# Optimization experiments

Measured on AMD Instinct MI355X. Metric: run time of the kernel, lower is better.

The kernel has to match this reference:

```python
import jax, jax.numpy as jnp
import numpy as np

N_SPK, N_UTT, D = 1024, 32, 128
EPS = 1e-8  # matches F.cosine_similarity eps


def setup_inputs() -> dict:
    key = jax.random.key(0)
    emb = jax.random.normal(key, (N_SPK * N_UTT, D), dtype=jnp.float32)
    emb = emb / jnp.linalg.norm(emb, axis=-1, keepdims=True)  # L2-normalized per docstring
    return {
        "embeddings": emb,
        "w": jnp.asarray(10.0, dtype=jnp.float32),
        "b": jnp.asarray(-5.0, dtype=jnp.float32),
        "n_speakers": N_SPK,
        "n_utterances": N_UTT,
    }


def reference(embeddings, w, b, n_speakers, n_utterances):
    # [N, M, D]
    e = embeddings.reshape(n_speakers, n_utterances, -1)
    cent = e.mean(axis=1)  # [N, D] full centroids
    # exclusive centroids: mean over all utterances except i -> [N, M, D]
    cent_excl = (e.sum(axis=1, keepdims=True) - e) / (n_utterances - 1)

    e_n = jnp.maximum(jnp.linalg.norm(e, axis=-1), EPS)          # [N, M]
    c_n = jnp.maximum(jnp.linalg.norm(cent, axis=-1), EPS)       # [N]
    ce_n = jnp.maximum(jnp.linalg.norm(cent_excl, axis=-1), EPS) # [N, M]

    # cosine sim of every utterance vs every full centroid: [N, M, N]
    sim = jnp.einsum('nmd,kd->nmk', e, cent) / (e_n[:, :, None] * c_n[None, None, :])
    # own-speaker entry uses the exclusive centroid instead
    sim_own = jnp.sum(e * cent_excl, axis=-1) / (e_n * ce_n)     # [N, M]
    eye = jnp.eye(n_speakers, dtype=bool)[:, None, :]            # [N, 1, N]
    sim = jnp.where(eye, sim_own[:, :, None], sim)

    logits = (w * sim + b).reshape(n_speakers * n_utterances, n_speakers)
    targets = jnp.repeat(jnp.arange(n_speakers), n_utterances)
    logp = jax.nn.log_softmax(logits, axis=-1)
    loss = -jnp.take_along_axis(logp, targets[:, None], axis=-1).mean()
    return loss
```

## Files before the change

### kernel.cpp

```cpp
#include <hip/hip_runtime.h>
#include <math.h>

#define NSPK 1024
#define NUTT 32
#define DIM  128
#define NROWS (NSPK * NUTT)
#define EPS 1e-8f
#define LOG2E 1.44269504f

typedef __attribute__((ext_vector_type(8))) short short8;
typedef __attribute__((ext_vector_type(4))) float floatx4;

__device__ inline unsigned short f2bf(float f) {
  union { float f; unsigned u; } v; v.f = f;
  unsigned r = v.u + 0x7fffu + ((v.u >> 16) & 1u);
  return (unsigned short)(r >> 16);
}

__global__ __launch_bounds__(256) void k_prep(const float* __restrict__ emb,
                                              const float* __restrict__ wp,
                                              const float* __restrict__ bp,
                                              unsigned short* __restrict__ centN,
                                              float* __restrict__ rs2,
                                              float* __restrict__ eol,
                                              float* __restrict__ olv) {
  __shared__ __align__(16) float E[32 * 132];
  __shared__ __align__(16) float Sl[128];
  __shared__ float red2[2];

  int n = blockIdx.x, t = threadIdx.x;

  const float4* e4 = (const float4*)emb + (size_t)n * 1024;
#pragma unroll
  for (int i = 0; i < 4; ++i) {
    int idx4 = t + 256 * i;
    int m = idx4 >> 5, d4 = (idx4 & 31) << 2;
    *(float4*)&E[m * 132 + d4] = e4[idx4];
  }
  __syncthreads();

  float s = 0.f;
  if (t < 128) {
    for (int m = 0; m < 32; ++m) s += E[m * 132 + t];
    Sl[t] = s;
    float p = s * s;
#pragma unroll
    for (int mask = 1; mask < 64; mask <<= 1) p += __shfl_xor(p, mask, 64);
    if ((t & 63) == 0) red2[t >> 6] = p;
  }
  __syncthreads();
  float ss = red2[0] + red2[1];

  if (t < 128) {
    float cn = fmaxf(sqrtf(ss) * (1.0f / NUTT), EPS);
    centN[(size_t)n * DIM + t] = f2bf(s / (NUTT * cn));
  }

  int row = t >> 3, sub = t & 7;
  float ee = 0.f, es = 0.f;
  int base = row * 132 + sub * 16;
#pragma unroll
  for (int i = 0; i < 4; ++i) {
    float4 ev = *(const float4*)&E[base + i * 4];
    float4 sv = *(const float4*)&Sl[sub * 16 + i * 4];
    ee += ev.x * ev.x + ev.y * ev.y + ev.z * ev.z + ev.w * ev.w;
    es += ev.x * sv.x + ev.y * sv.y + ev.z * sv.z + ev.w * sv.w;
  }
#pragma unroll
  for (int mask = 1; mask < 8; mask <<= 1) {
    ee += __shfl_xor(ee, mask, 64);
    es += __shfl_xor(es, mask, 64);
  }
  if (sub == 0) {
    float w = wp[0], b = bp[0];
    float M = b + fabsf(w);
    float en = fmaxf(sqrtf(ee), EPS);
    float dot_own = (es - ee) * (1.0f / (NUTT - 1));
    float ex2 = (ss - 2.0f * es + ee) * (1.0f / ((NUTT - 1) * (NUTT - 1)));
    float cen = fmaxf(sqrtf(ex2), EPS);
    float ol = w * dot_own / (en * cen) + b;
    int r = n * NUTT + row;
    olv[r] = ol;
    eol[r] = exp2f((ol - M) * LOG2E);
    rs2[r] = w * LOG2E / en;
  }
}

__global__ __launch_bounds__(256, 2) void k_mfma(const float* __restrict__ emb,
                                                 const unsigned short* __restrict__ centN,
                                                 const float* __restrict__ rs2g,
                                                 const float* __restrict__ eolg,
                                                 const float* __restrict__ olvg,
                                                 const float* __restrict__ wp,
                                                 const float* __restrict__ bp,
                                                 float* __restrict__ out) {
  __shared__ __align__(16) unsigned short A[64 * 136];
  __shared__ float sPart[4 * 64];

  int b = blockIdx.x, t = threadIdx.x;
  int wid = t >> 6, lane = t & 63;
  int lg = lane >> 4, lc = lane & 15;
  int s0 = b * 2;

  const float4* e4 = (const float4*)emb + (size_t)b * 2048;
#pragma unroll
  for (int i = 0; i < 8; ++i) {
    int idx4 = t + 256 * i;
    int lr = idx4 >> 5, d4 = (idx4 & 31) << 2;
    float4 v = e4[idx4];
    ushort4 bv;
    bv.x = f2bf(v.x); bv.y = f2bf(v.y); bv.z = f2bf(v.z); bv.w = f2bf(v.w);
    *(ushort4*)&A[lr * 136 + d4] = bv;
  }
  __syncthreads();

  short8 af[4][4];
#pragma unroll
  for (int rt = 0; rt < 4; ++rt)
#pragma unroll
    for (int ks = 0; ks < 4; ++ks)
      af[rt][ks] = *(const short8*)&A[(rt * 16 + lc) * 136 + ks * 32 + lg * 8];

  float rsL[16], eolL[16];
#pragma unroll
  for (int rt = 0; rt < 4; ++rt) {
    float4 r4 = *(const float4*)&rs2g[b * 64 + rt * 16 + lg * 4];
    float4 o4 = *(const float4*)&eolg[b * 64 + rt * 16 + lg * 4];
    rsL[rt * 4 + 0] = r4.x; rsL[rt * 4 + 1] = r4.y; rsL[rt * 4 + 2] = r4.z; rsL[rt * 4 + 3] = r4.w;
    eolL[rt * 4 + 0] = o4.x; eolL[rt * 4 + 1] = o4.y; eolL[rt * 4 + 2] = o4.z; eolL[rt * 4 + 3] = o4.w;
  }

  float w = wp[0], bb = bp[0];
  float M = bb + fabsf(w);
  float c2 = (bb - M) * LOG2E;

  float sAcc[16];
#pragma unroll
  for (int j = 0; j < 16; ++j) sAcc[j] = 0.f;

  int colbase = wid * 256;
#pragma unroll 2
  for (int ct = 0; ct < 16; ++ct) {
    int c0 = colbase + ct * 16;
    int col = c0 + lc;
    const short8* bptr = (const short8*)(centN + (size_t)col * DIM + lg * 8);
    short8 bf[4];
#pragma unroll
    for (int ks = 0; ks < 4; ++ks) bf[ks] = bptr[ks * 4];

    floatx4 acc[4];
#pragma unroll
    for (int rt = 0; rt < 4; ++rt) acc[rt] = (floatx4){0.f, 0.f, 0.f, 0.f};
#pragma unroll
    for (int ks = 0; ks < 4; ++ks)
#pragma unroll
      for (int rt = 0; rt < 4; ++rt)
        acc[rt] = __builtin_amdgcn_mfma_f32_16x16x32_bf16(af[rt][ks], bf[ks], acc[rt], 0, 0, 0);

    bool fix = (unsigned)(s0 - c0) < 16u;
#pragma unroll
    for (int rt = 0; rt < 4; ++rt) {
      int own = s0 + (rt >> 1);
#pragma unroll
      for (int reg = 0; reg < 4; ++reg) {
        float l2 = fmaf(rsL[rt * 4 + reg], acc[rt][reg], c2);
        float e = exp2f(l2);
        if (fix && col == own) e = eolL[rt * 4 + reg];
        sAcc[rt * 4 + reg] += e;
      }
    }
  }

#pragma unroll
  for (int mask = 1; mask < 16; mask <<= 1)
#pragma unroll
    for (int j = 0; j < 16; ++j) sAcc[j] += __shfl_xor(sAcc[j], mask, 64);

  if (lc == 0)
#pragma unroll
    for (int rt = 0; rt < 4; ++rt)
#pragma unroll
      for (int reg = 0; reg < 4; ++reg)
        sPart[wid * 64 + rt * 16 + lg * 4 + reg] = sAcc[rt * 4 + reg];
  __syncthreads();

  if (t < 64) {
    float st = sPart[t] + sPart[64 + t] + sPart[128 + t] + sPart[192 + t];
    float lossr = M + logf(st) - olvg[b * 64 + t];
#pragma unroll
    for (int mask = 1; mask < 64; mask <<= 1) lossr += __shfl_xor(lossr, mask, 64);
    if (t == 0) atomicAdd(out, lossr * (1.0f / NROWS));
  }
}

extern "C" void kernel_launch(void* const* d_in, const int* in_sizes, int n_in,
                              void* d_out, int out_size, void* d_ws, size_t ws_size,
                              hipStream_t stream) {
  const float* emb = (const float*)d_in[0];
  const float* wp  = (const float*)d_in[1];
  const float* bp  = (const float*)d_in[2];

  char* ws = (char*)d_ws;
  unsigned short* centN = (unsigned short*)ws;
  float* rs2 = (float*)(ws + 262144);
  float* eol = (float*)(ws + 262144 + 131072);
  float* olv = (float*)(ws + 262144 + 262144);
  float* out = (float*)d_out;

  hipMemsetAsync(d_out, 0, sizeof(float), stream);
  hipLaunchKernelGGL(k_prep, dim3(NSPK), dim3(256), 0, stream,
                     emb, wp, bp, centN, rs2, eol, olv);
  hipLaunchKernelGGL(k_mfma, dim3(NSPK / 2), dim3(256), 0, stream,
                     emb, centN, rs2, eol, olv, wp, bp, out);
}
```

Before: 98.25 us.

## Fuse prep and MFMA kernels into one cooperative launch with grid sync

Merges the centroid/prep kernel and the MFMA softmax kernel into a single cooperative kernel of 512 blocks. Each block preps its own two speakers, keeping per-row scalars and the bf16 A tile in shared memory, then grid-syncs before the similarity pass. A second grid sync replaces the memset and atomics with a deterministic final reduction. The B-fragment loads are also software-prefetched one column tile ahead. The aim is to remove launch gaps, the memset and the global round-trip of per-row data, at the cost of two grid-wide barriers and a startup probe with a fallback two-kernel path.

```diff
diff --git a/kernel.cpp b/kernel.cpp
--- a/kernel.cpp
+++ b/kernel.cpp
@@ -1,5 +1,8 @@
 #include <hip/hip_runtime.h>
+#include <hip/hip_cooperative_groups.h>
 #include <math.h>
+
+namespace cg = cooperative_groups;
 
 #define NSPK 1024
 #define NUTT 32
@@ -17,102 +20,82 @@
   return (unsigned short)(r >> 16);
 }
 
-__global__ __launch_bounds__(256) void k_prep(const float* __restrict__ emb,
-                                              const float* __restrict__ wp,
-                                              const float* __restrict__ bp,
-                                              unsigned short* __restrict__ centN,
-                                              float* __restrict__ rs2,
-                                              float* __restrict__ eol,
-                                              float* __restrict__ olv) {
-  __shared__ __align__(16) float E[32 * 132];
-  __shared__ __align__(16) float Sl[128];
-  __shared__ float red2[2];
-
-  int n = blockIdx.x, t = threadIdx.x;
-
-  const float4* e4 = (const float4*)emb + (size_t)n * 1024;
-#pragma unroll
-  for (int i = 0; i < 4; ++i) {
-    int idx4 = t + 256 * i;
-    int m = idx4 >> 5, d4 = (idx4 & 31) << 2;
-    *(float4*)&E[m * 132 + d4] = e4[idx4];
+__device__ __forceinline__ void phase1(
+    int b, int t, const float* __restrict__ emb, float w, float bb, float M,
+    unsigned short* __restrict__ centN, float* __restrict__ rs2g,
+    float* __restrict__ eolg, float* __restrict__ olvg,
+    float* Sl, float* red, float* rowRS, float* rowEOL, float* rowOLV,
+    unsigned short* A) {
+  int sp = t >> 7, d = t & 127;
+  {
+    const float* eb = emb + (size_t)(b * 2 + sp) * NUTT * DIM + d;
+    float s = 0.f;
+#pragma unroll
+    for (int m = 0; m < NUTT; ++m) s += eb[m * DIM];
+    Sl[sp * 128 + d] = s;
+    float p = s * s;
+#pragma unroll
+    for (int mask = 1; mask < 64; mask <<= 1) p += __shfl_xor(p, mask, 64);
+    if ((t & 63) == 0) red[t >> 6] = p;
   }
   __syncthreads();
-
-  float s = 0.f;
-  if (t < 128) {
-    for (int m = 0; m < 32; ++m) s += E[m * 132 + t];
-    Sl[t] = s;
-    float p = s * s;
-#pragma unroll
-    for (int mask = 1; mask < 64; mask <<= 1) p += __shfl_xor(p, mask, 64);
-    if ((t & 63) == 0) red2[t >> 6] = p;
-  }
-  __syncthreads();
-  float ss = red2[0] + red2[1];
-
-  if (t < 128) {
+  float ss0 = red[0] + red[1], ss1 = red[2] + red[3];
+
+  {
+    float ss = sp ? ss1 : ss0;
+    float s = Sl[sp * 128 + d];
     float cn = fmaxf(sqrtf(ss) * (1.0f / NUTT), EPS);
-    centN[(size_t)n * DIM + t] = f2bf(s / (NUTT * cn));
-  }
-
-  int row = t >> 3, sub = t & 7;
-  float ee = 0.f, es = 0.f;
-  int base = row * 132 + sub * 16;
-#pragma unroll
-  for (int i = 0; i < 4; ++i) {
-    float4 ev = *(const float4*)&E[base + i * 4];
-    float4 sv = *(const float4*)&Sl[sub * 16 + i * 4];
-    ee += ev.x * ev.x + ev.y * ev.y + ev.z * ev.z + ev.w * ev.w;
-    es += ev.x * sv.x + ev.y * sv.y + ev.z * sv.z + ev.w * sv.w;
-  }
-#pragma unroll
-  for (int mask = 1; mask < 8; mask <<= 1) {
-    ee += __shfl_xor(ee, mask, 64);
-    es += __shfl_xor(es, mask, 64);
-  }
-  if (sub == 0) {
-    float w = wp[0], b = bp[0];
-    float M = b + fabsf(w);
-    float en = fmaxf(sqrtf(ee), EPS);
-    float dot_own = (es - ee) * (1.0f / (NUTT - 1));
-    float ex2 = (ss - 2.0f * es + ee) * (1.0f / ((NUTT - 1) * (NUTT - 1)));
-    float cen = fmaxf(sqrtf(ex2), EPS);
-    float ol = w * dot_own / (en * cen) + b;
-    int r = n * NUTT + row;
-    olv[r] = ol;
-    eol[r] = exp2f((ol - M) * LOG2E);
-    rs2[r] = w * LOG2E / en;
-  }
-}
-
-__global__ __launch_bounds__(256, 2) void k_mfma(const float* __restrict__ emb,
-                                                 const unsigned short* __restrict__ centN,
-                                                 const float* __restrict__ rs2g,
-                                                 const float* __restrict__ eolg,
-                                                 const float* __restrict__ olvg,
-                                                 const float* __restrict__ wp,
-                                                 const float* __restrict__ bp,
-                                                 float* __restrict__ out) {
-  __shared__ __align__(16) unsigned short A[64 * 136];
-  __shared__ float sPart[4 * 64];
-
-  int b = blockIdx.x, t = threadIdx.x;
-  int wid = t >> 6, lane = t & 63;
-  int lg = lane >> 4, lc = lane & 15;
-  int s0 = b * 2;
-
-  const float4* e4 = (const float4*)emb + (size_t)b * 2048;
+    centN[(size_t)(b * 2 + sp) * DIM + d] = f2bf(s / (NUTT * cn));
+  }
+
+  {
+    int row = t >> 2, sub = t & 3;
+    int rsp = row >> 5;
+    const float* er = emb + (size_t)(b * 64 + row) * DIM + sub * 32;
+    const float* Srow = &Sl[rsp * 128 + sub * 32];
+    float ee = 0.f, es = 0.f;
+#pragma unroll
+    for (int i = 0; i < 8; ++i) {
+      float4 ev = *(const float4*)&er[i * 4];
+      float4 sv = *(const float4*)&Srow[i * 4];
+      ee += ev.x * ev.x + ev.y * ev.y + ev.z * ev.z + ev.w * ev.w;
+      es += ev.x * sv.x + ev.y * sv.y + ev.z * sv.z + ev.w * sv.w;
+    }
+    ee += __shfl_xor(ee, 1, 64); es += __shfl_xor(es, 1, 64);
+    ee += __shfl_xor(ee, 2, 64); es += __shfl_xor(es, 2, 64);
+    if (sub == 0) {
+      float ss = rsp ? ss1 : ss0;
+      float en = fmaxf(sqrtf(ee), EPS);
+      float dot_own = (es - ee) * (1.0f / (NUTT - 1));
+      float ex2 = (ss - 2.f * es + ee) * (1.0f / ((NUTT - 1) * (NUTT - 1)));
+      float cen = fmaxf(sqrtf(ex2), EPS);
+      float ol = w * dot_own / (en * cen) + bb;
+      float eo = exp2f((ol - M) * LOG2E);
+      float rs = w * LOG2E / en;
+      int gr = b * 64 + row;
+      rowOLV[row] = ol; olvg[gr] = ol;
+      rowEOL[row] = eo; eolg[gr] = eo;
+      rowRS[row] = rs;  rs2g[gr] = rs;
+    }
+  }
+
 #pragma unroll
   for (int i = 0; i < 8; ++i) {
     int idx4 = t + 256 * i;
-    int lr = idx4 >> 5, d4 = (idx4 & 31) << 2;
-    float4 v = e4[idx4];
+    int r = idx4 >> 5, d4 = (idx4 & 31) << 2;
+    float4 v = *(const float4*)(emb + (size_t)b * 8192 + (size_t)idx4 * 4);
     ushort4 bv;
     bv.x = f2bf(v.x); bv.y = f2bf(v.y); bv.z = f2bf(v.z); bv.w = f2bf(v.w);
-    *(ushort4*)&A[lr * 136 + d4] = bv;
-  }
-  __syncthreads();
+    *(ushort4*)&A[r * 136 + d4] = bv;
+  }
+}
+
+__device__ __forceinline__ float phase2(
+    int b, int t, const unsigned short* __restrict__ centN,
+    const unsigned short* A, const float* rowRS, const float* rowEOL,
+    const float* rowOLV, float M, float c2, float* sPart) {
+  int wid = t >> 6, lane = t & 63, lg = lane >> 4, lc = lane & 15;
+  int s0 = b * 2;
 
   short8 af[4][4];
 #pragma unroll
@@ -124,30 +107,31 @@
   float rsL[16], eolL[16];
 #pragma unroll
   for (int rt = 0; rt < 4; ++rt) {
-    float4 r4 = *(const float4*)&rs2g[b * 64 + rt * 16 + lg * 4];
-    float4 o4 = *(const float4*)&eolg[b * 64 + rt * 16 + lg * 4];
+    float4 r4 = *(const float4*)&rowRS[rt * 16 + lg * 4];
+    float4 o4 = *(const float4*)&rowEOL[rt * 16 + lg * 4];
     rsL[rt * 4 + 0] = r4.x; rsL[rt * 4 + 1] = r4.y; rsL[rt * 4 + 2] = r4.z; rsL[rt * 4 + 3] = r4.w;
     eolL[rt * 4 + 0] = o4.x; eolL[rt * 4 + 1] = o4.y; eolL[rt * 4 + 2] = o4.z; eolL[rt * 4 + 3] = o4.w;
   }
 
-  float w = wp[0], bb = bp[0];
-  float M = bb + fabsf(w);
-  float c2 = (bb - M) * LOG2E;
-
   float sAcc[16];
 #pragma unroll
   for (int j = 0; j < 16; ++j) sAcc[j] = 0.f;
 
   int colbase = wid * 256;
-#pragma unroll 2
+  int col0 = colbase + lc;
+  const short8* cb8 = (const short8*)centN;
+
+  short8 bcur[4], bnxt[4];
+  {
+    const short8* p = cb8 + (size_t)col0 * 16 + lg;
+    bcur[0] = p[0]; bcur[1] = p[4]; bcur[2] = p[8]; bcur[3] = p[12];
+  }
+
   for (int ct = 0; ct < 16; ++ct) {
-    int c0 = colbase + ct * 16;
-    int col = c0 + lc;
-    const short8* bptr = (const short8*)(centN + (size_t)col * DIM + lg * 8);
-    short8 bf[4];
-#pragma unroll
-    for (int ks = 0; ks < 4; ++ks) bf[ks] = bptr[ks * 4];
-
+    if (ct < 15) {
+      const short8* p = cb8 + (size_t)(col0 + (ct + 1) * 16) * 16 + lg;
+      bnxt[0] = p[0]; bnxt[1] = p[4]; bnxt[2] = p[8]; bnxt[3] = p[12];
+    }
     floatx4 acc[4];
 #pragma unroll
     for (int rt = 0; rt < 4; ++rt) acc[rt] = (floatx4){0.f, 0.f, 0.f, 0.f};
@@ -155,8 +139,9 @@
     for (int ks = 0; ks < 4; ++ks)
 #pragma unroll
       for (int rt = 0; rt < 4; ++rt)
-        acc[rt] = __builtin_amdgcn_mfma_f32_16x16x32_bf16(af[rt][ks], bf[ks], acc[rt], 0, 0, 0);
-
+        acc[rt] = __builtin_amdgcn_mfma_f32_16x16x32_bf16(af[rt][ks], bcur[ks], acc[rt], 0, 0, 0);
+
+    int c0 = colbase + ct * 16, col = c0 + lc;
     bool fix = (unsigned)(s0 - c0) < 16u;
 #pragma unroll
     for (int rt = 0; rt < 4; ++rt) {
@@ -169,6 +154,8 @@
         sAcc[rt * 4 + reg] += e;
       }
     }
+#pragma unroll
+    for (int ks = 0; ks < 4; ++ks) bcur[ks] = bnxt[ks];
   }
 
 #pragma unroll
@@ -184,13 +171,168 @@
         sPart[wid * 64 + rt * 16 + lg * 4 + reg] = sAcc[rt * 4 + reg];
   __syncthreads();
 
+  float blockSum = 0.f;
   if (t < 64) {
     float st = sPart[t] + sPart[64 + t] + sPart[128 + t] + sPart[192 + t];
-    float lossr = M + logf(st) - olvg[b * 64 + t];
+    float lossr = M + logf(st) - rowOLV[t];
 #pragma unroll
     for (int mask = 1; mask < 64; mask <<= 1) lossr += __shfl_xor(lossr, mask, 64);
-    if (t == 0) atomicAdd(out, lossr * (1.0f / NROWS));
-  }
+    blockSum = lossr;
+  }
+  return blockSum;
+}
+
+__global__ __launch_bounds__(256, 2) void k_fused(const float* __restrict__ emb,
+                                                  const float* __restrict__ wp,
+                                                  const float* __restrict__ bp,
+                                                  unsigned short* __restrict__ centN,
+                                                  float* __restrict__ rs2g,
+                                                  float* __restrict__ eolg,
+                                                  float* __restrict__ olvg,
+                                                  float* __restrict__ partial,
+                                                  float* __restrict__ out) {
+  __shared__ __align__(16) unsigned short A[64 * 136];
+  __shared__ __align__(16) float Sl[2 * 128];
+  __shared__ float red[4];
+  __shared__ __align__(16) float rowRS[64], rowEOL[64], rowOLV[64];
+  __shared__ __align__(16) float sPart[256];
+
+  int b = blockIdx.x, t = threadIdx.x;
+  float w = wp[0], bb = bp[0];
+  float M = bb + fabsf(w);
+  float c2 = -fabsf(w) * LOG2E;
+
+  phase1(b, t, emb, w, bb, M, centN, rs2g, eolg, olvg,
+         Sl, red, rowRS, rowEOL, rowOLV, A);
+
+  __threadfence();
+  cg::this_grid().sync();
+
+  float v = phase2(b, t, centN, A, rowRS, rowEOL, rowOLV, M, c2, sPart);
+  if (t == 0) partial[b] = v;
+
+  __threadfence();
+  cg::this_grid().sync();
+
+  if (b == 0) {
+    float s = partial[t] + partial[t + 256];
+#pragma unroll
+    for (int mask = 1; mask < 64; mask <<= 1) s += __shfl_xor(s, mask, 64);
+    __syncthreads();
+    if ((t & 63) == 0) red[t >> 6] = s;
+    __syncthreads();
+    if (t == 0) out[0] = (red[0] + red[1] + red[2] + red[3]) * (1.0f / NROWS);
+  }
+}
+
+__global__ __launch_bounds__(256) void k_prep_fb(const float* __restrict__ emb,
+                                                 const float* __restrict__ wp,
+                                                 const float* __restrict__ bp,
+                                                 unsigned short* __restrict__ centN,
+                                                 float* __restrict__ rs2g,
+                                                 float* __restrict__ eolg,
+                                                 float* __restrict__ olvg,
+                                                 float* __restrict__ out) {
+  __shared__ __align__(16) unsigned short A[64 * 136];
+  __shared__ __align__(16) float Sl[2 * 128];
+  __shared__ float red[4];
+  __shared__ __align__(16) float rowRS[64], rowEOL[64], rowOLV[64];
+  int b = blockIdx.x, t = threadIdx.x;
+  float w = wp[0], bb = bp[0];
+  float M = bb + fabsf(w);
+  if (b == 0 && t == 0) out[0] = 0.f;
+  phase1(b, t, emb, w, bb, M, centN, rs2g, eolg, olvg,
+         Sl, red, rowRS, rowEOL, rowOLV, A);
+}
+
+__global__ __launch_bounds__(256, 2) void k_mfma_fb(const float* __restrict__ emb,
+                                                    const unsigned short* __restrict__ centN,
+                                                    const float* __restrict__ rs2g,
+                                                    const float* __restrict__ eolg,
+                                                    const float* __restrict__ olvg,
+                                                    const float* __restrict__ wp,
+                                                    const float* __restrict__ bp,
+                                                    float* __restrict__ out) {
+  __shared__ __align__(16) unsigned short A[64 * 136];
+  __shared__ __align__(16) float rowRS[64], rowEOL[64], rowOLV[64];
+  __shared__ __align__(16) float sPart[256];
+
+  int b = blockIdx.x, t = threadIdx.x;
+  float w = wp[0], bb = bp[0];
+  float M = bb + fabsf(w);
+  float c2 = -fabsf(w) * LOG2E;
+
+#pragma unroll
+  for (int i = 0; i < 8; ++i) {
+    int idx4 = t + 256 * i;
+    int r = idx4 >> 5, d4 = (idx4 & 31) << 2;
+    float4 v = *(const float4*)(emb + (size_t)b * 8192 + (size_t)idx4 * 4);
+    ushort4 bv;
+    bv.x = f2bf(v.x); bv.y = f2bf(v.y); bv.z = f2bf(v.z); bv.w = f2bf(v.w);
+    *(ushort4*)&A[r * 136 + d4] = bv;
+  }
+  if (t < 64) {
+    rowRS[t] = rs2g[b * 64 + t];
+    rowEOL[t] = eolg[b * 64 + t];
+    rowOLV[t] = olvg[b * 64 + t];
+  }
+  __syncthreads();
+
+  float v = phase2(b, t, centN, A, rowRS, rowEOL, rowOLV, M, c2, sPart);
+  if (t == 0) atomicAdd(out, v * (1.0f / NROWS));
+}
+
+static int g_use_coop = 0;
+
+__global__ void k_coop_probe(int* flag) {
+  cg::this_grid().sync();
+  if (blockIdx.x == 0 && threadIdx.x == 0) flag[0] = 123;
+}
+
+namespace {
+struct CoopInit {
+  CoopInit() {
+    int dev = 0;
+    if (hipGetDevice(&dev) != hipSuccess) return;
+    hipDeviceProp_t prop;
+    if (hipGetDeviceProperties(&prop, dev) != hipSuccess) return;
+    if (!prop.cooperativeLaunch) return;
+    int maxb = 0;
+    if (hipOccupancyMaxActiveBlocksPerMultiprocessor(&maxb, k_fused, 256, 0) != hipSuccess) return;
+    if ((long long)maxb * prop.multiProcessorCount < 512) return;
+
+    int* dflag = nullptr;
+    if (hipMalloc(&dflag, sizeof(int)) != hipSuccess) return;
+    hipMemset(dflag, 0, sizeof(int));
+    hipStream_t s = nullptr;
+    if (hipStreamCreate(&s) != hipSuccess) { hipFree(dflag); return; }
+
+    bool ok = true;
+    if (hipStreamBeginCapture(s, hipStreamCaptureModeRelaxed) != hipSuccess) ok = false;
+    hipGraph_t g = nullptr;
+    hipGraphExec_t ge = nullptr;
+    if (ok) {
+      void* args[] = {(void*)&dflag};
+      if (hipLaunchCooperativeKernel((const void*)k_coop_probe, dim3(2), dim3(64),
+                                     args, 0, s) != hipSuccess) ok = false;
+      if (hipStreamEndCapture(s, &g) != hipSuccess || g == nullptr) ok = false;
+      if (ok && hipGraphInstantiate(&ge, g, nullptr, nullptr, 0) != hipSuccess) ok = false;
+      if (ok && hipGraphLaunch(ge, s) != hipSuccess) ok = false;
+      if (hipStreamSynchronize(s) != hipSuccess) ok = false;
+      if (ok) {
+        int h = 0;
+        hipMemcpy(&h, dflag, sizeof(int), hipMemcpyDeviceToHost);
+        if (h != 123) ok = false;
+      }
+    }
+    if (ge) hipGraphExecDestroy(ge);
+    if (g) hipGraphDestroy(g);
+    hipStreamDestroy(s);
+    hipFree(dflag);
+    g_use_coop = ok ? 1 : 0;
+  }
+};
+static CoopInit g_init;
 }
 
 extern "C" void kernel_launch(void* const* d_in, const int* in_sizes, int n_in,
@@ -202,14 +344,22 @@
 
   char* ws = (char*)d_ws;
   unsigned short* centN = (unsigned short*)ws;
-  float* rs2 = (float*)(ws + 262144);
-  float* eol = (float*)(ws + 262144 + 131072);
-  float* olv = (float*)(ws + 262144 + 262144);
+  float* partial = (float*)(ws + 262144);
+  float* rs2g = (float*)(ws + 262144 + 4096);
+  float* eolg = (float*)(ws + 262144 + 4096 + 131072);
+  float* olvg = (float*)(ws + 262144 + 4096 + 262144);
   float* out = (float*)d_out;
 
-  hipMemsetAsync(d_out, 0, sizeof(float), stream);
-  hipLaunchKernelGGL(k_prep, dim3(NSPK), dim3(256), 0, stream,
-                     emb, wp, bp, centN, rs2, eol, olv);
-  hipLaunchKernelGGL(k_mfma, dim3(NSPK / 2), dim3(256), 0, stream,
-                     emb, centN, rs2, eol, olv, wp, bp, out);
-}
+  if (g_use_coop) {
+    void* args[] = {(void*)&emb, (void*)&wp, (void*)&bp, (void*)&centN,
+                    (void*)&rs2g, (void*)&eolg, (void*)&olvg,
+                    (void*)&partial, (void*)&out};
+    hipLaunchCooperativeKernel((const void*)k_fused, dim3(512), dim3(256),
+                               args, 0, stream);
+  } else {
+    hipLaunchKernelGGL(k_prep_fb, dim3(512), dim3(256), 0, stream,
+                       emb, wp, bp, centN, rs2g, eolg, olvg, out);
+    hipLaunchKernelGGL(k_mfma_fb, dim3(512), dim3(256), 0, stream,
+                       emb, centN, rs2g, eolg, olvg, wp, bp, out);
+  }
+}
```

After: 95.39 us. 2.9% less time.
